# Kernel optimization log

Hardware: AMD Instinct MI355X
Metric: run time of the kernel (lower is better)

The kernel has to match this reference:

```python
import jax, jax.numpy as jnp
import numpy as np

FACTOR = 8
IN_DIM = 4096
OUT_DIM = 4096


def setup_inputs() -> dict:
    key = jax.random.key(0)
    kx, ka, ks = jax.random.split(key, 3)
    x = jax.random.normal(kx, (4, 2048, IN_DIM), dtype=jnp.float32)
    a = jax.random.normal(ka, (FACTOR, FACTOR, FACTOR), dtype=jnp.float32) * 0.1
    s = jax.random.normal(ks, (FACTOR, OUT_DIM // FACTOR, IN_DIM // FACTOR), dtype=jnp.float32) * 0.05
    return {"x": x, "a": a, "s": s}


def reference(x, a, s):
    f = a.shape[0]
    out_dim = a.shape[1] * s.shape[1]
    in_dim = a.shape[2] * s.shape[2]
    # Batched Kronecker product: (f, a_rows*k, a_cols*p) then sum over batch dim f.
    # weight[a*k + ?, c*p + ?] = sum_b a[b, ar, ac] * s[b, kr, pc]
    p = jnp.einsum('bac,bkp->bakcp', a, s)  # (f, f, out/f, f, in/f)
    weight = p.reshape(f, out_dim, in_dim).sum(axis=0)  # (out, in)
    return x @ weight.T
```

## Files before the change

### kernel.cpp

```cpp
#include <hip/hip_runtime.h>
#include <hip/hip_bf16.h>
#include <stdint.h>

namespace {

constexpr int MTOT = 8192;
constexpr int NTOT = 4096;
constexpr int KTOT = 4096;

constexpr int BM = 256, BN = 256, BK = 32;
constexpr int NT = KTOT / BK;

constexpr int CONV_BLOCKS = (MTOT * KTOT / 8) / 256;
constexpr int GENW_BLOCKS = (NTOT * KTOT / 8) / 256;

typedef __attribute__((ext_vector_type(8))) short bf16x8;
typedef __attribute__((ext_vector_type(4))) float f32x4;

__device__ inline unsigned short to_bf16(float f) {
    union { float f; uint32_t u; } v; v.f = f;
    return (unsigned short)((v.u + 0x7FFFu + ((v.u >> 16) & 1u)) >> 16);
}

__global__ __launch_bounds__(256) void prep_kernel(const float* __restrict__ x,
                                                   const float* __restrict__ a,
                                                   const float* __restrict__ s,
                                                   unsigned short* __restrict__ xb,
                                                   unsigned short* __restrict__ wb) {
    if (blockIdx.x < CONV_BLOCKS) {
        int idx = blockIdx.x * 256 + threadIdx.x;
        const f32x4* xv = reinterpret_cast<const f32x4*>(x);
        f32x4 v0 = xv[2 * idx];
        f32x4 v1 = xv[2 * idx + 1];
        union { bf16x8 v; unsigned short q[8]; } o;
        o.q[0] = to_bf16(v0.x); o.q[1] = to_bf16(v0.y);
        o.q[2] = to_bf16(v0.z); o.q[3] = to_bf16(v0.w);
        o.q[4] = to_bf16(v1.x); o.q[5] = to_bf16(v1.y);
        o.q[6] = to_bf16(v1.z); o.q[7] = to_bf16(v1.w);
        reinterpret_cast<bf16x8*>(xb)[idx] = o.v;
    } else {
        int idx = (blockIdx.x - CONV_BLOCKS) * 256 + threadIdx.x;
        int o  = idx >> 9;
        int i8 = idx & 511;
        int i0 = i8 * 8;
        int obig = o >> 9, orow = o & 511;
        int ibig = i0 >> 9, icol = i0 & 511;

        float acc[8];
#pragma unroll
        for (int j = 0; j < 8; ++j) acc[j] = 0.f;
#pragma unroll
        for (int b = 0; b < 8; ++b) {
            float av = a[b * 64 + obig * 8 + ibig];
            const f32x4* sv = reinterpret_cast<const f32x4*>(s + b * 512 * 512 + orow * 512 + icol);
            f32x4 s0 = sv[0], s1 = sv[1];
            acc[0] += av * s0.x; acc[1] += av * s0.y; acc[2] += av * s0.z; acc[3] += av * s0.w;
            acc[4] += av * s1.x; acc[5] += av * s1.y; acc[6] += av * s1.z; acc[7] += av * s1.w;
        }
        union { bf16x8 v; unsigned short q[8]; } ov;
#pragma unroll
        for (int j = 0; j < 8; ++j) ov.q[j] = to_bf16(acc[j]);
        reinterpret_cast<bf16x8*>(wb)[idx] = ov.v;
    }
}

__global__ __launch_bounds__(512, 2)
void gemm_bt_kernel(const unsigned short* __restrict__ A,
                    const unsigned short* __restrict__ B,
                    float* __restrict__ C) {
    __shared__ __align__(16) unsigned short As[4][BM][BK];
    __shared__ __align__(16) unsigned short Bs[4][BN][BK];

    int bid = blockIdx.x;
    int swz = (bid & 7) * 64 + (bid >> 3);
    int bm = swz >> 4;
    int bn = swz & 15;

    int tid  = threadIdx.x;
    int wid  = tid >> 6;
    int lane = tid & 63;
    int wm = wid >> 2, wn = wid & 3;

    int srow  = lane >> 2;
    int sslot = (lane & 3) ^ ((srow >> 1) & 3);
    const unsigned short* ag0 = A + (size_t)(bm * BM + wid * 16 + srow) * KTOT + sslot * 8;
    const unsigned short* ag1 = ag0 + (size_t)128 * KTOT;
    const unsigned short* bg0 = B + (size_t)(bn * BN + wid * 16 + srow) * KTOT + sslot * 8;
    const unsigned short* bg1 = bg0 + (size_t)128 * KTOT;

    int rl    = lane & 15;
    int rslot = (lane >> 4) ^ ((rl >> 1) & 3);

    f32x4 acc[8][4];
#pragma unroll
    for (int m = 0; m < 8; ++m)
#pragma unroll
        for (int n = 0; n < 4; ++n) acc[m][n] = (f32x4)0.f;

    auto STAGE_A = [&](int s, int k0) {
        __builtin_amdgcn_global_load_lds(
            (const __attribute__((address_space(1))) void*)(ag0 + k0),
            (__attribute__((address_space(3))) void*)&As[s][wid * 16][0], 16, 0, 0);
        __builtin_amdgcn_global_load_lds(
            (const __attribute__((address_space(1))) void*)(ag1 + k0),
            (__attribute__((address_space(3))) void*)&As[s][128 + wid * 16][0], 16, 0, 0);
    };
    auto STAGE_B = [&](int s, int k0) {
        __builtin_amdgcn_global_load_lds(
            (const __attribute__((address_space(1))) void*)(bg0 + k0),
            (__attribute__((address_space(3))) void*)&Bs[s][wid * 16][0], 16, 0, 0);
        __builtin_amdgcn_global_load_lds(
            (const __attribute__((address_space(1))) void*)(bg1 + k0),
            (__attribute__((address_space(3))) void*)&Bs[s][128 + wid * 16][0], 16, 0, 0);
    };

    auto LDA = [&](int s, int mi) -> bf16x8 {
        return *reinterpret_cast<const bf16x8*>(&As[s][wm * 128 + mi * 16 + rl][rslot * 8]);
    };
    auto LDB = [&](int s, int ni) -> bf16x8 {
        return *reinterpret_cast<const bf16x8*>(&Bs[s][wn * 64 + ni * 16 + rl][rslot * 8]);
    };

    bf16x8 fa[4], fb[4], ga[4], pa[4], pb[4];

    STAGE_A(0, 0);          STAGE_B(0, 0);
    STAGE_A(1, BK);         STAGE_B(1, BK);
    STAGE_A(2, 2 * BK);     STAGE_B(2, 2 * BK);
    asm volatile("s_waitcnt vmcnt(4)" ::: "memory");
    __builtin_amdgcn_s_barrier();
#pragma unroll
    for (int m = 0; m < 4; ++m) fa[m] = LDA(0, m);
#pragma unroll
    for (int n = 0; n < 4; ++n) fb[n] = LDB(0, n);

    for (int tb = 0; tb < NT; tb += 4) {
#pragma unroll
        for (int u = 0; u < 4; ++u) {
            const int t  = tb + u;
            const int s  = u;
            const int nx = (u + 1) & 3;
            const int ss = (u + 3) & 3;
            const bool st = (t + 3) < NT;
            const int k0 = (t + 3) * BK;

#pragma unroll
            for (int m = 0; m < 4; ++m) ga[m] = LDA(s, m + 4);
            if (st) STAGE_A(ss, k0);
            asm volatile("s_waitcnt lgkmcnt(4)" ::: "memory");
            __builtin_amdgcn_sched_barrier(0);
            __builtin_amdgcn_s_setprio(1);
#pragma unroll
            for (int m = 0; m < 4; ++m)
#pragma unroll
                for (int n = 0; n < 4; ++n)
                    acc[m][n] = __builtin_amdgcn_mfma_f32_16x16x32_bf16(fa[m], fb[n], acc[m][n], 0, 0, 0);
            __builtin_amdgcn_s_setprio(0);

#pragma unroll
            for (int m = 0; m < 4; ++m) pa[m] = LDA(nx, m);
#pragma unroll
            for (int n = 0; n < 4; ++n) pb[n] = LDB(nx, n);
            if (st) STAGE_B(ss, k0);
            asm volatile("s_waitcnt lgkmcnt(8)" ::: "memory");
            __builtin_amdgcn_sched_barrier(0);
            __builtin_amdgcn_s_setprio(1);
#pragma unroll
            for (int m = 0; m < 4; ++m)
#pragma unroll
                for (int n = 0; n < 4; ++n)
                    acc[m + 4][n] = __builtin_amdgcn_mfma_f32_16x16x32_bf16(ga[m], fb[n], acc[m + 4][n], 0, 0, 0);
            __builtin_amdgcn_s_setprio(0);

            asm volatile("s_waitcnt vmcnt(4)" ::: "memory");
            __builtin_amdgcn_s_barrier();

#pragma unroll
            for (int m = 0; m < 4; ++m) fa[m] = pa[m];
#pragma unroll
            for (int n = 0; n < 4; ++n) fb[n] = pb[n];
        }
    }

    int crow0 = bm * BM + wm * 128 + (lane >> 4) * 4;
    int ccol0 = bn * BN + wn * 64 + (lane & 15);
#pragma unroll
    for (int m = 0; m < 8; ++m)
#pragma unroll
        for (int n = 0; n < 4; ++n)
#pragma unroll
            for (int j = 0; j < 4; ++j) {
                size_t r = (size_t)(crow0 + m * 16 + j);
                size_t c = (size_t)(ccol0 + n * 16);
                C[r * NTOT + c] = acc[m][n][j];
            }
}

}

extern "C" void kernel_launch(void* const* d_in, const int* in_sizes, int n_in,
                              void* d_out, int out_size, void* d_ws, size_t ws_size,
                              hipStream_t stream) {
    const float* x = (const float*)d_in[0];
    const float* a = (const float*)d_in[1];
    const float* s = (const float*)d_in[2];
    float* out = (float*)d_out;

    unsigned short* xb = (unsigned short*)d_ws;
    unsigned short* wb = xb + (size_t)MTOT * KTOT;

    prep_kernel<<<CONV_BLOCKS + GENW_BLOCKS, 256, 0, stream>>>(x, a, s, xb, wb);
    gemm_bt_kernel<<<(MTOT / 256) * (NTOT / 256), 512, 0, stream>>>(xb, wb, out);
}
```

Measured before the change: 289.8 us.

## Restructure GEMM mainloop into BK=64 half-tile ping-pong with fine-grained staging

```diff
diff --git a/kernel.cpp b/kernel.cpp
--- a/kernel.cpp
+++ b/kernel.cpp
@@ -7,9 +7,6 @@
 constexpr int MTOT = 8192;
 constexpr int NTOT = 4096;
 constexpr int KTOT = 4096;
-
-constexpr int BM = 256, BN = 256, BK = 32;
-constexpr int NT = KTOT / BK;
 
 constexpr int CONV_BLOCKS = (MTOT * KTOT / 8) / 256;
 constexpr int GENW_BLOCKS = (NTOT * KTOT / 8) / 256;
@@ -45,7 +42,6 @@
         int i0 = i8 * 8;
         int obig = o >> 9, orow = o & 511;
         int ibig = i0 >> 9, icol = i0 & 511;
-
         float acc[8];
 #pragma unroll
         for (int j = 0; j < 8; ++j) acc[j] = 0.f;
@@ -68,8 +64,8 @@
 void gemm_bt_kernel(const unsigned short* __restrict__ A,
                     const unsigned short* __restrict__ B,
                     float* __restrict__ C) {
-    __shared__ __align__(16) unsigned short As[4][BM][BK];
-    __shared__ __align__(16) unsigned short Bs[4][BN][BK];
+    __shared__ __align__(16) unsigned short As[2][2][128][64];
+    __shared__ __align__(16) unsigned short Bs[2][2][128][64];
 
     int bid = blockIdx.x;
     int swz = (bid & 7) * 64 + (bid >> 3);
@@ -81,15 +77,44 @@
     int lane = tid & 63;
     int wm = wid >> 2, wn = wid & 3;
 
-    int srow  = lane >> 2;
-    int sslot = (lane & 3) ^ ((srow >> 1) & 3);
-    const unsigned short* ag0 = A + (size_t)(bm * BM + wid * 16 + srow) * KTOT + sslot * 8;
-    const unsigned short* ag1 = ag0 + (size_t)128 * KTOT;
-    const unsigned short* bg0 = B + (size_t)(bn * BN + wid * 16 + srow) * KTOT + sslot * 8;
-    const unsigned short* bg1 = bg0 + (size_t)128 * KTOT;
-
-    int rl    = lane & 15;
-    int rslot = (lane >> 4) ^ ((rl >> 1) & 3);
+    int sr = lane >> 3;
+    int su = (lane & 7) ^ sr;
+    const size_t K = (size_t)KTOT;
+    const unsigned short* Ag = A + (size_t)(bm * 256 + wid * 16 + sr) * K + su * 8;
+    const unsigned short* Bg = B + (size_t)(bn * 256 + wid * 16 + sr) * K + su * 8;
+
+    auto SA = [&](int buf, int h, int tile) {
+        const unsigned short* src = Ag + (size_t)(h * 128) * K + tile * 64;
+        __builtin_amdgcn_global_load_lds(
+            (const __attribute__((address_space(1))) void*)src,
+            (__attribute__((address_space(3))) void*)&As[buf][h][wid * 16][0], 16, 0, 0);
+        __builtin_amdgcn_global_load_lds(
+            (const __attribute__((address_space(1))) void*)(src + 8 * K),
+            (__attribute__((address_space(3))) void*)&As[buf][h][wid * 16 + 8][0], 16, 0, 0);
+    };
+    auto SB = [&](int buf, int h, int tile) {
+        const unsigned short* src = Bg + (size_t)(h * 128) * K + tile * 64;
+        __builtin_amdgcn_global_load_lds(
+            (const __attribute__((address_space(1))) void*)src,
+            (__attribute__((address_space(3))) void*)&Bs[buf][h][wid * 16][0], 16, 0, 0);
+        __builtin_amdgcn_global_load_lds(
+            (const __attribute__((address_space(1))) void*)(src + 8 * K),
+            (__attribute__((address_space(3))) void*)&Bs[buf][h][wid * 16 + 8][0], 16, 0, 0);
+    };
+
+    int rl = lane & 15;
+    int kq = lane >> 4;
+    int rx = rl & 7;
+    auto LDA = [&](int buf, int mq, int i, int ks) -> bf16x8 {
+        int row = mq * 64 + i * 16 + rl;
+        int u = (ks * 4 + kq) ^ rx;
+        return *reinterpret_cast<const bf16x8*>(&As[buf][wm][row][u * 8]);
+    };
+    auto LDB = [&](int buf, int nq, int gi, int ks) -> bf16x8 {
+        int row = (wn & 1) * 64 + nq * 32 + gi * 16 + rl;
+        int u = (ks * 4 + kq) ^ rx;
+        return *reinterpret_cast<const bf16x8*>(&Bs[buf][wn >> 1][row][u * 8]);
+    };
 
     f32x4 acc[8][4];
 #pragma unroll
@@ -97,101 +122,113 @@
 #pragma unroll
         for (int n = 0; n < 4; ++n) acc[m][n] = (f32x4)0.f;
 
-    auto STAGE_A = [&](int s, int k0) {
-        __builtin_amdgcn_global_load_lds(
-            (const __attribute__((address_space(1))) void*)(ag0 + k0),
-            (__attribute__((address_space(3))) void*)&As[s][wid * 16][0], 16, 0, 0);
-        __builtin_amdgcn_global_load_lds(
-            (const __attribute__((address_space(1))) void*)(ag1 + k0),
-            (__attribute__((address_space(3))) void*)&As[s][128 + wid * 16][0], 16, 0, 0);
-    };
-    auto STAGE_B = [&](int s, int k0) {
-        __builtin_amdgcn_global_load_lds(
-            (const __attribute__((address_space(1))) void*)(bg0 + k0),
-            (__attribute__((address_space(3))) void*)&Bs[s][wid * 16][0], 16, 0, 0);
-        __builtin_amdgcn_global_load_lds(
-            (const __attribute__((address_space(1))) void*)(bg1 + k0),
-            (__attribute__((address_space(3))) void*)&Bs[s][128 + wid * 16][0], 16, 0, 0);
-    };
-
-    auto LDA = [&](int s, int mi) -> bf16x8 {
-        return *reinterpret_cast<const bf16x8*>(&As[s][wm * 128 + mi * 16 + rl][rslot * 8]);
-    };
-    auto LDB = [&](int s, int ni) -> bf16x8 {
-        return *reinterpret_cast<const bf16x8*>(&Bs[s][wn * 64 + ni * 16 + rl][rslot * 8]);
-    };
-
-    bf16x8 fa[4], fb[4], ga[4], pa[4], pb[4];
-
-    STAGE_A(0, 0);          STAGE_B(0, 0);
-    STAGE_A(1, BK);         STAGE_B(1, BK);
-    STAGE_A(2, 2 * BK);     STAGE_B(2, 2 * BK);
-    asm volatile("s_waitcnt vmcnt(4)" ::: "memory");
+    bf16x8 af[4][2], b0[2][2], b1[2][2];
+
+    auto MM = [&](int mq, int nq, bf16x8 (&bq)[2][2]) {
+        __builtin_amdgcn_s_setprio(1);
+#pragma unroll
+        for (int i = 0; i < 4; ++i)
+#pragma unroll
+            for (int gi = 0; gi < 2; ++gi)
+#pragma unroll
+                for (int ks = 0; ks < 2; ++ks)
+                    acc[mq * 4 + i][nq * 2 + gi] = __builtin_amdgcn_mfma_f32_16x16x32_bf16(
+                        af[i][ks], bq[gi][ks], acc[mq * 4 + i][nq * 2 + gi], 0, 0, 0);
+        __builtin_amdgcn_s_setprio(0);
+        __builtin_amdgcn_s_barrier();
+    };
+
+    SB(0, 0, 0); SB(0, 1, 0); SA(0, 0, 0); SA(0, 1, 0);
+    SB(1, 0, 1); SB(1, 1, 1);
+    asm volatile("s_waitcnt vmcnt(0)" ::: "memory");
     __builtin_amdgcn_s_barrier();
-#pragma unroll
-    for (int m = 0; m < 4; ++m) fa[m] = LDA(0, m);
-#pragma unroll
-    for (int n = 0; n < 4; ++n) fb[n] = LDB(0, n);
-
-    for (int tb = 0; tb < NT; tb += 4) {
-#pragma unroll
-        for (int u = 0; u < 4; ++u) {
-            const int t  = tb + u;
-            const int s  = u;
-            const int nx = (u + 1) & 3;
-            const int ss = (u + 3) & 3;
-            const bool st = (t + 3) < NT;
-            const int k0 = (t + 3) * BK;
-
-#pragma unroll
-            for (int m = 0; m < 4; ++m) ga[m] = LDA(s, m + 4);
-            if (st) STAGE_A(ss, k0);
-            asm volatile("s_waitcnt lgkmcnt(4)" ::: "memory");
-            __builtin_amdgcn_sched_barrier(0);
-            __builtin_amdgcn_s_setprio(1);
-#pragma unroll
-            for (int m = 0; m < 4; ++m)
-#pragma unroll
-                for (int n = 0; n < 4; ++n)
-                    acc[m][n] = __builtin_amdgcn_mfma_f32_16x16x32_bf16(fa[m], fb[n], acc[m][n], 0, 0, 0);
-            __builtin_amdgcn_s_setprio(0);
-
-#pragma unroll
-            for (int m = 0; m < 4; ++m) pa[m] = LDA(nx, m);
-#pragma unroll
-            for (int n = 0; n < 4; ++n) pb[n] = LDB(nx, n);
-            if (st) STAGE_B(ss, k0);
-            asm volatile("s_waitcnt lgkmcnt(8)" ::: "memory");
-            __builtin_amdgcn_sched_barrier(0);
-            __builtin_amdgcn_s_setprio(1);
-#pragma unroll
-            for (int m = 0; m < 4; ++m)
-#pragma unroll
-                for (int n = 0; n < 4; ++n)
-                    acc[m + 4][n] = __builtin_amdgcn_mfma_f32_16x16x32_bf16(ga[m], fb[n], acc[m + 4][n], 0, 0, 0);
-            __builtin_amdgcn_s_setprio(0);
-
-            asm volatile("s_waitcnt vmcnt(4)" ::: "memory");
-            __builtin_amdgcn_s_barrier();
-
-#pragma unroll
-            for (int m = 0; m < 4; ++m) fa[m] = pa[m];
-#pragma unroll
-            for (int n = 0; n < 4; ++n) fb[n] = pb[n];
-        }
+
+    for (int j = 0; j < 32; ++j) {
+        const int t1 = 2 * j + 1;
+        const int te = (2 * j + 2 > 62) ? 62 : 2 * j + 2;
+        const int to = (2 * j + 3 > 63) ? 63 : 2 * j + 3;
+
+#pragma unroll
+        for (int i = 0; i < 4; ++i) { af[i][0] = LDA(0, 0, i, 0); af[i][1] = LDA(0, 0, i, 1); }
+#pragma unroll
+        for (int gi = 0; gi < 2; ++gi) { b0[gi][0] = LDB(0, 0, gi, 0); b0[gi][1] = LDB(0, 0, gi, 1); }
+        SA(1, 0, t1);
+        asm volatile("s_waitcnt lgkmcnt(8)" ::: "memory");
+        __builtin_amdgcn_s_barrier();
+        asm volatile("s_waitcnt lgkmcnt(0)" ::: "memory");
+        __builtin_amdgcn_sched_barrier(0);
+        MM(0, 0, b0);
+
+#pragma unroll
+        for (int gi = 0; gi < 2; ++gi) { b1[gi][0] = LDB(0, 1, gi, 0); b1[gi][1] = LDB(0, 1, gi, 1); }
+        SA(1, 1, t1);
+        __builtin_amdgcn_s_barrier();
+        asm volatile("s_waitcnt lgkmcnt(0)" ::: "memory");
+        __builtin_amdgcn_sched_barrier(0);
+        MM(0, 1, b1);
+
+#pragma unroll
+        for (int i = 0; i < 4; ++i) { af[i][0] = LDA(0, 1, i, 0); af[i][1] = LDA(0, 1, i, 1); }
+        SB(0, 0, te);
+        __builtin_amdgcn_s_barrier();
+        asm volatile("s_waitcnt lgkmcnt(0)" ::: "memory");
+        __builtin_amdgcn_sched_barrier(0);
+        MM(1, 0, b0);
+
+        SB(0, 1, te);
+        asm volatile("s_waitcnt vmcnt(4)" ::: "memory");
+        __builtin_amdgcn_s_barrier();
+        asm volatile("s_waitcnt lgkmcnt(0)" ::: "memory");
+        __builtin_amdgcn_sched_barrier(0);
+        MM(1, 1, b1);
+
+#pragma unroll
+        for (int i = 0; i < 4; ++i) { af[i][0] = LDA(1, 0, i, 0); af[i][1] = LDA(1, 0, i, 1); }
+#pragma unroll
+        for (int gi = 0; gi < 2; ++gi) { b0[gi][0] = LDB(1, 0, gi, 0); b0[gi][1] = LDB(1, 0, gi, 1); }
+        SA(0, 0, te);
+        asm volatile("s_waitcnt lgkmcnt(8)" ::: "memory");
+        __builtin_amdgcn_s_barrier();
+        asm volatile("s_waitcnt lgkmcnt(0)" ::: "memory");
+        __builtin_amdgcn_sched_barrier(0);
+        MM(0, 0, b0);
+
+#pragma unroll
+        for (int gi = 0; gi < 2; ++gi) { b1[gi][0] = LDB(1, 1, gi, 0); b1[gi][1] = LDB(1, 1, gi, 1); }
+        SA(0, 1, te);
+        __builtin_amdgcn_s_barrier();
+        asm volatile("s_waitcnt lgkmcnt(0)" ::: "memory");
+        __builtin_amdgcn_sched_barrier(0);
+        MM(0, 1, b1);
+
+#pragma unroll
+        for (int i = 0; i < 4; ++i) { af[i][0] = LDA(1, 1, i, 0); af[i][1] = LDA(1, 1, i, 1); }
+        SB(1, 0, to);
+        __builtin_amdgcn_s_barrier();
+        asm volatile("s_waitcnt lgkmcnt(0)" ::: "memory");
+        __builtin_amdgcn_sched_barrier(0);
+        MM(1, 0, b0);
+
+        SB(1, 1, to);
+        asm volatile("s_waitcnt vmcnt(4)" ::: "memory");
+        __builtin_amdgcn_s_barrier();
+        asm volatile("s_waitcnt lgkmcnt(0)" ::: "memory");
+        __builtin_amdgcn_sched_barrier(0);
+        MM(1, 1, b1);
     }
-
-    int crow0 = bm * BM + wm * 128 + (lane >> 4) * 4;
-    int ccol0 = bn * BN + wn * 64 + (lane & 15);
+    asm volatile("s_waitcnt vmcnt(0)" ::: "memory");
+
+    int crow0 = bm * 256 + wm * 128 + (lane >> 4) * 4;
+    int ccol0 = bn * 256 + wn * 64 + (lane & 15);
 #pragma unroll
     for (int m = 0; m < 8; ++m)
 #pragma unroll
         for (int n = 0; n < 4; ++n)
 #pragma unroll
-            for (int j = 0; j < 4; ++j) {
-                size_t r = (size_t)(crow0 + m * 16 + j);
+            for (int jj = 0; jj < 4; ++jj) {
+                size_t r = (size_t)(crow0 + m * 16 + jj);
                 size_t c = (size_t)(ccol0 + n * 16);
-                C[r * NTOT + c] = acc[m][n][j];
+                C[r * NTOT + c] = acc[m][n][jj];
             }
 }
 
```

New measurement: 322.1 us. +11.1%, slower.
